# Kernel optimization log

Hardware: AMD Instinct MI355X
Metric: run time of the kernel (lower is better)

Reference implementation:

```python
import jax, jax.numpy as jnp
import numpy as np

B, C, H, W = 16, 256, 128, 128
INTER = C // 2  # NLBlockND default inter_channels = in_channels // 2
BN_EPS = 1e-5


def setup_inputs() -> dict:
    key = jax.random.key(0)
    ks = jax.random.split(key, 14)
    s = lambda n: 1.0 / np.sqrt(n)
    inp = {
        'x':  jax.random.normal(ks[0], (B, C, H, W), jnp.float32),
        # NLBlockND 1x1 convs (spatial input is 1x1 after avg-pool -> matmuls)
        'Wg': jax.random.normal(ks[1], (INTER, C), jnp.float32) * s(C),
        'bg': jax.random.normal(ks[2], (INTER,), jnp.float32) * s(C),
        'Wt': jax.random.normal(ks[3], (INTER, C), jnp.float32) * s(C),
        'bt': jax.random.normal(ks[4], (INTER,), jnp.float32) * s(C),
        'Wp': jax.random.normal(ks[5], (INTER, C), jnp.float32) * s(C),
        'bp': jax.random.normal(ks[6], (INTER,), jnp.float32) * s(C),
        'Wf': jax.random.normal(ks[7], (1, 2 * INTER), jnp.float32) * s(2 * INTER),
        'bf': jax.random.normal(ks[8], (1,), jnp.float32) * s(2 * INTER),
        'Wz': jax.random.normal(ks[9], (C, INTER), jnp.float32) * s(INTER),
        'bz': jax.random.normal(ks[10], (C,), jnp.float32) * s(INTER),
        'gamma': jax.random.normal(ks[11], (C,), jnp.float32),
        'beta':  jax.random.normal(ks[12], (C,), jnp.float32),
        # eca_layer_two: Conv2d(C, 1, kernel_size=1, bias=False)
        'W3': jax.random.normal(ks[13], (1, C), jnp.float32) * s(C),
    }
    return inp


def reference(x, Wg, bg, Wt, bt, Wp, bp, Wf, bf, Wz, bz, gamma, beta, W3):
    b = x.shape[0]
    # ---- nonlocal_layer: avg-pool -> NLBlockND('concatenate') on 1x1 map ----
    p = jnp.mean(x, axis=(2, 3))                      # [b, C] pooled vector
    g_x = p @ Wg.T + bg                               # [b, INTER]
    th  = p @ Wt.T + bt                               # theta  [b, INTER]
    ph  = p @ Wp.T + bp                               # phi    [b, INTER]
    cat = jnp.concatenate([th, ph], axis=1)           # [b, 2*INTER]
    f = jax.nn.relu(cat @ Wf.T + bf)                  # [b, 1]; N=1 so f_div_C = f
    y = f * g_x                                       # [b, INTER]
    wy = y @ Wz.T + bz                                # [b, C]
    # BatchNorm2d (training mode, spatial=1x1): stats over batch per channel
    mu = jnp.mean(wy, axis=0)
    var = jnp.var(wy, axis=0)
    bn = gamma * (wy - mu) * jax.lax.rsqrt(var + BN_EPS) + beta
    z = bn + p                                        # residual
    scores = jax.nn.sigmoid(z)                        # [b, C]
    # top-3 channel selection, then per-sample gather of channels from x
    _, idx = jax.lax.top_k(scores, 3)                 # [b, 3]
    x1 = jnp.take_along_axis(x, idx[:, :, None, None], axis=1)  # [b, 3, H, W]
    # ---- eca_layer_two: 1x1 conv C->1 (no bias) + exact GELU ----
    x3 = jax.nn.gelu(jnp.einsum('bchw,oc->bohw', x, W3), approximate=False)  # [b,1,H,W]
    # conv2 (eca_layer_one) output is discarded (x2 = zeros_like, unused)
    return jnp.concatenate([x3, x1], axis=1)          # [b, 4, H, W]
```

## Files before the change

kernel.cpp:

```cpp
#include <hip/hip_runtime.h>

#define HW    16384
#define NCH   256
#define NB    16
#define INTER 128
#define HW4   4096
#define WSTR  34
#define NT    32


__global__ __launch_bounds__(512, 2) void k_pool_x3(
    const float* __restrict__ x, const float* __restrict__ W3, float* out)
{
    const int tile = blockIdx.x;
    const int b    = blockIdx.y;
    const int tid  = threadIdx.x;
    const int wave = tid >> 6, lane = tid & 63;
    const int c0   = wave << 5;

    __shared__ float  w3f[NCH];
    __shared__ float  wsum[NCH * WSTR];
    __shared__ float4 comb[8][128];

    if (tid < NCH) w3f[tid] = W3[tid];
    __syncthreads();

    const float4* xb = (const float4*)x + (size_t)b * NCH * HW4
                     + (size_t)c0 * HW4 + tile * 128 + lane;

    float4 a0 = make_float4(0.f, 0.f, 0.f, 0.f);
    float4 a1 = make_float4(0.f, 0.f, 0.f, 0.f);

    float4 bufA[4], bufB[4];
    #pragma unroll
    for (int j = 0; j < 4; ++j)
        bufA[j] = xb[(size_t)(j >> 1) * HW4 + (j & 1) * 64];

    #define PROCESS(BUF, CBASE)                                             \
        _Pragma("unroll")                                                   \
        for (int h = 0; h < 2; ++h) {                                       \
            const int c = (CBASE) + h;                                      \
            const float w = w3f[c0 + c];                                    \
            float4 v0 = BUF[h * 2], v1 = BUF[h * 2 + 1];                    \
            a0.x = fmaf(v0.x, w, a0.x); a0.y = fmaf(v0.y, w, a0.y);         \
            a0.z = fmaf(v0.z, w, a0.z); a0.w = fmaf(v0.w, w, a0.w);         \
            a1.x = fmaf(v1.x, w, a1.x); a1.y = fmaf(v1.y, w, a1.y);         \
            a1.z = fmaf(v1.z, w, a1.z); a1.w = fmaf(v1.w, w, a1.w);         \
            float cs = ((v0.x + v0.y) + (v0.z + v0.w))                      \
                     + ((v1.x + v1.y) + (v1.z + v1.w));                     \
            cs += __shfl_xor(cs, 32);                                       \
            if (lane < 32) wsum[(c0 + c) * WSTR + lane] = cs;               \
        }

    for (int cc = 0; cc < 32; cc += 4) {
        #pragma unroll
        for (int j = 0; j < 4; ++j)
            bufB[j] = xb[(size_t)(cc + 2 + (j >> 1)) * HW4 + (j & 1) * 64];
        PROCESS(bufA, cc)
        if (cc + 4 < 32) {
            #pragma unroll
            for (int j = 0; j < 4; ++j)
                bufA[j] = xb[(size_t)(cc + 4 + (j >> 1)) * HW4 + (j & 1) * 64];
        }
        PROCESS(bufB, cc + 2)
    }
    #undef PROCESS

    comb[wave][lane]      = a0;
    comb[wave][64 + lane] = a1;
    __syncthreads();

    {
        const int ch = tid >> 1, half = tid & 1;
        const float* rowp = &wsum[ch * WSTR + half * 16];
        float s = 0.f;
        #pragma unroll
        for (int k = 0; k < 8; ++k) {
            float2 v2 = *(const float2*)(rowp + k * 2);
            s += v2.x + v2.y;
        }
        s += __shfl_xor(s, 1);
        if (half == 0)
            out[(size_t)(b * 4 + 1) * HW + tile * NCH + ch] = s;
    }

    if (tid < 128) {
        float4 v = comb[0][tid];
        #pragma unroll
        for (int j = 1; j < 8; ++j) {
            float4 u = comb[j][tid];
            v.x += u.x; v.y += u.y; v.z += u.z; v.w += u.w;
        }
        const float is2 = 0.70710678118654752440f;
        float4 r;
        r.x = 0.5f * v.x * (1.f + erff(v.x * is2));
        r.y = 0.5f * v.y * (1.f + erff(v.y * is2));
        r.z = 0.5f * v.z * (1.f + erff(v.z * is2));
        r.w = 0.5f * v.w * (1.f + erff(v.w * is2));
        ((float4*)out)[(size_t)b * 4 * HW4 + tile * 128 + tid] = r;
    }
}

__global__ __launch_bounds__(256) void k_mlp(
    const float* outbuf,
    const float* __restrict__ Wg, const float* __restrict__ bg,
    const float* __restrict__ Wt, const float* __restrict__ bt,
    const float* __restrict__ Wp, const float* __restrict__ bp,
    const float* __restrict__ Wf, const float* __restrict__ bfv,
    const float* __restrict__ Wz, const float* __restrict__ bz,
    float* __restrict__ p_out, float* __restrict__ wy_out)
{
    const int b = blockIdx.x, tid = threadIdx.x;
    __shared__ float sp[NCH];
    __shared__ float sg[INTER], sth[INTER], sph[INTER];
    __shared__ float red[NCH];
    __shared__ float sy[INTER];
    __shared__ float sf;

    const float* psum = outbuf + (size_t)(b * 4 + 1) * HW;
    float s = 0.f;
    #pragma unroll
    for (int t = 0; t < NT; ++t) s += psum[t * NCH + tid];
    float pv = s * (1.0f / 16384.0f);
    sp[tid] = pv;
    p_out[b * NCH + tid] = pv;
    __syncthreads();

    for (int j = tid; j < 3 * INTER; j += 256) {
        const float* Wrow; float bias; int i, which;
        if (j < INTER)        { i = j;           Wrow = Wg + i * NCH; bias = bg[i]; which = 0; }
        else if (j < 2*INTER) { i = j - INTER;   Wrow = Wt + i * NCH; bias = bt[i]; which = 1; }
        else                  { i = j - 2*INTER; Wrow = Wp + i * NCH; bias = bp[i]; which = 2; }
        float acc = bias;
        for (int k = 0; k < NCH; k += 4) {
            float4 q = *(const float4*)(Wrow + k);
            acc = fmaf(q.x, sp[k+0], acc);
            acc = fmaf(q.y, sp[k+1], acc);
            acc = fmaf(q.z, sp[k+2], acc);
            acc = fmaf(q.w, sp[k+3], acc);
        }
        if (which == 0) sg[i] = acc;
        else if (which == 1) sth[i] = acc;
        else sph[i] = acc;
    }
    __syncthreads();

    float cat = (tid < INTER) ? sth[tid] : sph[tid - INTER];
    red[tid] = cat * Wf[tid];
    __syncthreads();
    if (tid == 0) {
        float acc = bfv[0];
        for (int k = 0; k < NCH; ++k) acc += red[k];
        sf = fmaxf(acc, 0.f);
    }
    __syncthreads();
    if (tid < INTER) sy[tid] = sf * sg[tid];
    __syncthreads();

    {
        const float* Wrow = Wz + tid * INTER;
        float acc = bz[tid];
        for (int k = 0; k < INTER; k += 4) {
            float4 q = *(const float4*)(Wrow + k);
            acc = fmaf(q.x, sy[k+0], acc);
            acc = fmaf(q.y, sy[k+1], acc);
            acc = fmaf(q.z, sy[k+2], acc);
            acc = fmaf(q.w, sy[k+3], acc);
        }
        wy_out[b * NCH + tid] = acc;
    }
}

__global__ __launch_bounds__(256) void k_bn_topk(
    const float* __restrict__ wy, const float* __restrict__ p,
    const float* __restrict__ gamma, const float* __restrict__ beta,
    int* __restrict__ sel_out)
{
    const int b = blockIdx.x, tid = threadIdx.x;
    const int wave = tid >> 6, lane = tid & 63;
    __shared__ float wsc[4];
    __shared__ int   wid[4];
    __shared__ int   sel[3];

    float vv[16];
    float mu = 0.f;
    #pragma unroll
    for (int bb = 0; bb < 16; ++bb) { vv[bb] = wy[bb * NCH + tid]; mu += vv[bb]; }
    mu *= (1.f / 16.f);
    float var = 0.f;
    #pragma unroll
    for (int bb = 0; bb < 16; ++bb) { float d = vv[bb] - mu; var = fmaf(d, d, var); }
    var *= (1.f / 16.f);

    float bn = gamma[tid] * (vv[b] - mu) * rsqrtf(var + 1e-5f) + beta[tid];
    float z  = bn + p[b * NCH + tid];
    float sc = 1.f / (1.f + expf(-z));

    for (int r = 0; r < 3; ++r) {
        float s = sc; int id = tid;
        #pragma unroll
        for (int m = 1; m <= 32; m <<= 1) {
            float so = __shfl_xor(s, m);
            int   io = __shfl_xor(id, m);
            if (so > s || (so == s && io < id)) { s = so; id = io; }
        }
        if (lane == 0) { wsc[wave] = s; wid[wave] = id; }
        __syncthreads();
        if (tid == 0) {
            float bs = wsc[0]; int bi = wid[0];
            for (int w = 1; w < 4; ++w)
                if (wsc[w] > bs || (wsc[w] == bs && wid[w] < bi)) { bs = wsc[w]; bi = wid[w]; }
            sel[r] = bi;
        }
        __syncthreads();
        if (tid == sel[r]) sc = -1e30f;
        __syncthreads();
    }
    if (tid < 3) sel_out[b * 3 + tid] = sel[tid];
}

__global__ __launch_bounds__(256) void k_gather(
    const float* __restrict__ x, const int* __restrict__ sel,
    float* __restrict__ out)
{
    const int seg = blockIdx.x;
    const int r   = blockIdx.y;
    const int b   = blockIdx.z;
    const int ch  = sel[b * 3 + r];
    const float4* src = (const float4*)x + (size_t)(b * NCH + ch) * HW4 + seg * 1024;
    float4*       dst = (float4*)out + (size_t)(b * 4 + 1 + r) * HW4 + seg * 1024;
    #pragma unroll
    for (int i = 0; i < 4; ++i)
        dst[i * 256 + threadIdx.x] = src[i * 256 + threadIdx.x];
}

extern "C" void kernel_launch(void* const* d_in, const int* in_sizes, int n_in,
                              void* d_out, int out_size, void* d_ws, size_t ws_size,
                              hipStream_t stream)
{
    const float* x     = (const float*)d_in[0];
    const float* Wg    = (const float*)d_in[1];
    const float* bg    = (const float*)d_in[2];
    const float* Wt    = (const float*)d_in[3];
    const float* bt    = (const float*)d_in[4];
    const float* Wp    = (const float*)d_in[5];
    const float* bp    = (const float*)d_in[6];
    const float* Wf    = (const float*)d_in[7];
    const float* bfv   = (const float*)d_in[8];
    const float* Wz    = (const float*)d_in[9];
    const float* bz    = (const float*)d_in[10];
    const float* gamma = (const float*)d_in[11];
    const float* beta  = (const float*)d_in[12];
    const float* W3    = (const float*)d_in[13];
    float* out = (float*)d_out;

    float* wy  = (float*)d_ws;
    float* p   = wy + NB * NCH;
    int*   sel = (int*)(p + NB * NCH);

    k_pool_x3<<<dim3(NT, 16), 512, 0, stream>>>(x, W3, out);
    k_mlp<<<NB, 256, 0, stream>>>(out, Wg, bg, Wt, bt, Wp, bp, Wf, bfv, Wz, bz, p, wy);
    k_bn_topk<<<NB, 256, 0, stream>>>(wy, p, gamma, beta, sel);
    k_gather<<<dim3(4, 3, NB), 256, 0, stream>>>(x, sel, out);
}
```

Measured before the change: 432.5 us.

## Double pooling tile width and use triple-buffered register prefetch pipeline

The pool/x3 kernel now handles 256 float4 columns per block instead of 128, which halves the number of tiles. The channel loop is replaced with a fully unrolled three-buffer register pipeline that keeps two stages of 8 float4 loads in flight. The goal is more outstanding memory traffic per wave and fewer blocks, to better hide global load latency. In exchange it raises register pressure under the 512x2 launch bound, so spills are possible, and the grid shrinks to 256 blocks, which may leave CUs underused.

```diff
diff --git a/kernel.cpp b/kernel.cpp
--- a/kernel.cpp
+++ b/kernel.cpp
@@ -6,7 +6,7 @@
 #define INTER 128
 #define HW4   4096
 #define WSTR  34
-#define NT    32
+#define NT    16
 
 
 __global__ __launch_bounds__(512, 2) void k_pool_x3(
@@ -20,54 +20,61 @@
 
     __shared__ float  w3f[NCH];
     __shared__ float  wsum[NCH * WSTR];
-    __shared__ float4 comb[8][128];
+    __shared__ float4 comb[8][256];
 
     if (tid < NCH) w3f[tid] = W3[tid];
     __syncthreads();
 
     const float4* xb = (const float4*)x + (size_t)b * NCH * HW4
-                     + (size_t)c0 * HW4 + tile * 128 + lane;
-
-    float4 a0 = make_float4(0.f, 0.f, 0.f, 0.f);
-    float4 a1 = make_float4(0.f, 0.f, 0.f, 0.f);
-
-    float4 bufA[4], bufB[4];
-    #pragma unroll
-    for (int j = 0; j < 4; ++j)
-        bufA[j] = xb[(size_t)(j >> 1) * HW4 + (j & 1) * 64];
-
-    #define PROCESS(BUF, CBASE)                                             \
+                     + (size_t)c0 * HW4 + tile * 256 + lane;
+
+    float4 a[4];
+    #pragma unroll
+    for (int q = 0; q < 4; ++q) a[q] = make_float4(0.f, 0.f, 0.f, 0.f);
+
+    float4 R0[8], R1[8], R2[8];
+
+    #define LOAD(R, BT)                                                     \
+        _Pragma("unroll")                                                   \
+        for (int j = 0; j < 8; ++j)                                         \
+            R[j] = xb[(size_t)((BT) * 2 + (j >> 2)) * HW4 + (j & 3) * 64];
+
+    #define PROC(R, BT)                                                     \
         _Pragma("unroll")                                                   \
         for (int h = 0; h < 2; ++h) {                                       \
-            const int c = (CBASE) + h;                                      \
+            const int c = (BT) * 2 + h;                                     \
             const float w = w3f[c0 + c];                                    \
-            float4 v0 = BUF[h * 2], v1 = BUF[h * 2 + 1];                    \
-            a0.x = fmaf(v0.x, w, a0.x); a0.y = fmaf(v0.y, w, a0.y);         \
-            a0.z = fmaf(v0.z, w, a0.z); a0.w = fmaf(v0.w, w, a0.w);         \
-            a1.x = fmaf(v1.x, w, a1.x); a1.y = fmaf(v1.y, w, a1.y);         \
-            a1.z = fmaf(v1.z, w, a1.z); a1.w = fmaf(v1.w, w, a1.w);         \
-            float cs = ((v0.x + v0.y) + (v0.z + v0.w))                      \
-                     + ((v1.x + v1.y) + (v1.z + v1.w));                     \
+            float cs = 0.f;                                                 \
+            _Pragma("unroll")                                               \
+            for (int q = 0; q < 4; ++q) {                                   \
+                float4 v = R[h * 4 + q];                                    \
+                a[q].x = fmaf(v.x, w, a[q].x);                              \
+                a[q].y = fmaf(v.y, w, a[q].y);                              \
+                a[q].z = fmaf(v.z, w, a[q].z);                              \
+                a[q].w = fmaf(v.w, w, a[q].w);                              \
+                cs += (v.x + v.y) + (v.z + v.w);                            \
+            }                                                               \
             cs += __shfl_xor(cs, 32);                                       \
             if (lane < 32) wsum[(c0 + c) * WSTR + lane] = cs;               \
         }
 
-    for (int cc = 0; cc < 32; cc += 4) {
-        #pragma unroll
-        for (int j = 0; j < 4; ++j)
-            bufB[j] = xb[(size_t)(cc + 2 + (j >> 1)) * HW4 + (j & 1) * 64];
-        PROCESS(bufA, cc)
-        if (cc + 4 < 32) {
-            #pragma unroll
-            for (int j = 0; j < 4; ++j)
-                bufA[j] = xb[(size_t)(cc + 4 + (j >> 1)) * HW4 + (j & 1) * 64];
-        }
-        PROCESS(bufB, cc + 2)
-    }
-    #undef PROCESS
-
-    comb[wave][lane]      = a0;
-    comb[wave][64 + lane] = a1;
+    #define STEP(I, RP, RL)                                                 \
+        { if ((I) + 2 < 16) { LOAD(RL, (I) + 2) } PROC(RP, I) }
+
+    LOAD(R0, 0)
+    LOAD(R1, 1)
+    STEP( 0, R0, R2)  STEP( 1, R1, R0)  STEP( 2, R2, R1)
+    STEP( 3, R0, R2)  STEP( 4, R1, R0)  STEP( 5, R2, R1)
+    STEP( 6, R0, R2)  STEP( 7, R1, R0)  STEP( 8, R2, R1)
+    STEP( 9, R0, R2)  STEP(10, R1, R0)  STEP(11, R2, R1)
+    STEP(12, R0, R2)  STEP(13, R1, R0)  STEP(14, R2, R1)
+    STEP(15, R0, R2)
+    #undef STEP
+    #undef PROC
+    #undef LOAD
+
+    #pragma unroll
+    for (int q = 0; q < 4; ++q) comb[wave][q * 64 + lane] = a[q];
     __syncthreads();
 
     {
@@ -84,7 +91,7 @@
             out[(size_t)(b * 4 + 1) * HW + tile * NCH + ch] = s;
     }
 
-    if (tid < 128) {
+    if (tid < 256) {
         float4 v = comb[0][tid];
         #pragma unroll
         for (int j = 1; j < 8; ++j) {
@@ -97,7 +104,7 @@
         r.y = 0.5f * v.y * (1.f + erff(v.y * is2));
         r.z = 0.5f * v.z * (1.f + erff(v.z * is2));
         r.w = 0.5f * v.w * (1.f + erff(v.w * is2));
-        ((float4*)out)[(size_t)b * 4 * HW4 + tile * 128 + tid] = r;
+        ((float4*)out)[(size_t)b * 4 * HW4 + tile * 256 + tid] = r;
     }
 }
 
```

New measurement: 514.3 us. 18.9% more time.
